# Kernel optimization log

Measured on AMD Instinct MI355X. Metric: run time of the kernel, lower is better.

## Reference

```python
import jax, jax.numpy as jnp
import numpy as np

T = 512        # sequence / max_length
I = 512        # input_dim
H = 1024       # hidden_size
O = 1          # output_size
L = 512        # max_length (attention logits)


def setup_inputs() -> dict:
    key = jax.random.key(0)
    ks = jax.random.split(key, 14)
    s = 0.02
    return {
        "input_seq": jax.random.normal(ks[0], (T, I), jnp.float32),
        "target_seq": jax.random.normal(ks[1], (T, O), jnp.float32),
        # encoder LSTM (input I -> hidden H), PyTorch gate order i,f,g,o
        "W_ih_e": jax.random.normal(ks[2], (4 * H, I), jnp.float32) * s,
        "W_hh_e": jax.random.normal(ks[3], (4 * H, H), jnp.float32) * s,
        "b_ih_e": jnp.zeros((4 * H,), jnp.float32),
        "b_hh_e": jnp.zeros((4 * H,), jnp.float32),
        # attention: Linear(2H -> L)
        "W_attn": jax.random.normal(ks[4], (L, 2 * H), jnp.float32) * s,
        "b_attn": jnp.zeros((L,), jnp.float32),
        # decoder LSTM (input 2H -> hidden H)
        "W_ih_d": jax.random.normal(ks[5], (4 * H, 2 * H), jnp.float32) * s,
        "W_hh_d": jax.random.normal(ks[6], (4 * H, H), jnp.float32) * s,
        "b_ih_d": jnp.zeros((4 * H,), jnp.float32),
        "b_hh_d": jnp.zeros((4 * H,), jnp.float32),
        # output Linear(H -> O)
        "W_out": jax.random.normal(ks[7], (O, H), jnp.float32) * s,
        "b_out": jnp.zeros((O,), jnp.float32),
    }


def _lstm_cell(x, h, c, Wih, Whh, bih, bhh):
    gates = Wih @ x + bih + Whh @ h + bhh          # [4H]
    i, f, g, o = jnp.split(gates, 4)
    c = jax.nn.sigmoid(f) * c + jax.nn.sigmoid(i) * jnp.tanh(g)
    h = jax.nn.sigmoid(o) * jnp.tanh(c)
    return h, c


def reference(input_seq, target_seq, W_ih_e, W_hh_e, b_ih_e, b_hh_e,
              W_attn, b_attn, W_ih_d, W_hh_d, b_ih_d, b_hh_d, W_out, b_out):
    Th = input_seq.shape[0]
    max_len = W_attn.shape[0]
    hid = W_hh_e.shape[1]

    def step(carry, xs):
        eh, ec, dh, dc, aw = carry
        x_t, i = xs
        eh, ec = _lstm_cell(x_t, eh, ec, W_ih_e, W_hh_e, b_ih_e, b_hh_e)
        energy = W_attn @ jnp.concatenate([eh, dh]) + b_attn   # [L]
        aw = aw.at[i].set(energy[i])
        aw = jax.nn.softmax(aw)                                 # re-softmaxed each step, as in source
        context = aw[i] * eh                                    # [H]
        din = jnp.concatenate([context, dh])                    # [2H]
        dh, dc = _lstm_cell(din, dh, dc, W_ih_d, W_hh_d, b_ih_d, b_hh_d)
        out_t = W_out @ dh + b_out                              # [O]
        return (eh, ec, dh, dc, aw), out_t

    z = jnp.zeros((hid,), input_seq.dtype)
    carry0 = (z, z, z, z, jnp.zeros((max_len,), input_seq.dtype))
    _, output_seq = jax.lax.scan(step, carry0, (input_seq, jnp.arange(Th)))
    return output_seq  # [T, O]
```

## Files before the change

kernel.cpp:

```cpp
#include <hip/hip_runtime.h>
#include <math.h>


#define T_STEPS 512
#define ENC_BLK 128
#define NBLK    256
#define NTHR    512
#define POLL_LIMIT 30000u

typedef float fv4 __attribute__((ext_vector_type(4)));

__device__ __forceinline__ float sigf(float x) { return 1.0f / (1.0f + expf(-x)); }

__device__ __forceinline__ void st_bypass4(float* p, float v) {
  asm volatile("global_store_dword %0, %1, off sc0 sc1"
               :: "v"(p), "v"(v) : "memory");
}

__device__ __forceinline__ bool valid4(fv4 v) {
  return __float_as_uint(v.x) != 0xAAAAAAAAu && __float_as_uint(v.y) != 0xAAAAAAAAu &&
         __float_as_uint(v.z) != 0xAAAAAAAAu && __float_as_uint(v.w) != 0xAAAAAAAAu;
}

__device__ __forceinline__ fv4 poll2(const float* p, int* okp) {
  fv4 a, b;
  int ok = 1;
  asm volatile("global_load_dwordx4 %0, %1, off sc0 sc1" : "=v"(a) : "v"(p) : "memory");
  for (unsigned it = 0;; ++it) {
    asm volatile("global_load_dwordx4 %0, %1, off sc0 sc1" : "=v"(b) : "v"(p) : "memory");
    asm volatile("s_waitcnt vmcnt(1)" : "+v"(a) :: "memory");
    if (valid4(a)) { asm volatile("s_waitcnt vmcnt(0)" ::: "memory"); break; }
    asm volatile("global_load_dwordx4 %0, %1, off sc0 sc1" : "=v"(a) : "v"(p) : "memory");
    asm volatile("s_waitcnt vmcnt(1)" : "+v"(b) :: "memory");
    if (valid4(b)) { asm volatile("s_waitcnt vmcnt(0)" ::: "memory"); a = b; break; }
    if (it > POLL_LIMIT) { ok = 0; asm volatile("s_waitcnt vmcnt(0)" ::: "memory"); break; }
  }
  *okp = ok;
  return a;
}

__global__ __launch_bounds__(256) void prep_gemm(const float* __restrict__ X,
                                                 const float* __restrict__ Wih,
                                                 const float* __restrict__ bih,
                                                 const float* __restrict__ bhh,
                                                 float* __restrict__ px) {
  __shared__ float Ws[64][68];
  __shared__ float Xs[64][68];
  const int r0 = blockIdx.x * 64;
  const int t0 = blockIdx.y * 64;
  const int tid = threadIdx.x;
  const int tr = tid & 15;
  const int tc = tid >> 4;
  float acc[4][4] = {{0.f}};
  for (int k0 = 0; k0 < 512; k0 += 64) {
    __syncthreads();
    const int lr = tid >> 4;
    const int lc = (tid & 15) * 4;
#pragma unroll
    for (int rep = 0; rep < 4; rep++) {
      const int row = lr + rep * 16;
      const float4 wv = *(const float4*)&Wih[(size_t)(r0 + row) * 512 + k0 + lc];
      Ws[lc + 0][row] = wv.x; Ws[lc + 1][row] = wv.y;
      Ws[lc + 2][row] = wv.z; Ws[lc + 3][row] = wv.w;
      const float4 xv = *(const float4*)&X[(size_t)(t0 + row) * 512 + k0 + lc];
      Xs[row][lc + 0] = xv.x; Xs[row][lc + 1] = xv.y;
      Xs[row][lc + 2] = xv.z; Xs[row][lc + 3] = xv.w;
    }
    __syncthreads();
    for (int kk = 0; kk < 64; kk++) {
      float a[4], x[4];
#pragma unroll
      for (int i = 0; i < 4; i++) a[i] = Ws[kk][tr * 4 + i];
#pragma unroll
      for (int j = 0; j < 4; j++) x[j] = Xs[tc * 4 + j][kk];
#pragma unroll
      for (int i = 0; i < 4; i++)
#pragma unroll
        for (int j = 0; j < 4; j++) acc[i][j] += a[i] * x[j];
    }
  }
#pragma unroll
  for (int i = 0; i < 4; i++) {
    const int r = r0 + tr * 4 + i;
    const int g = r >> 10, h = r & 1023;
    const float bsum = bih[r] + bhh[r];
#pragma unroll
    for (int j = 0; j < 4; j++) {
      const int t = t0 + tc * 4 + j;
      px[((size_t)t * 1024 + h) * 4 + g] = acc[i][j] + bsum;
    }
  }
}

__global__ __launch_bounds__(512, 1) void lstm_persist(
    const float* __restrict__ Whhe, const float* __restrict__ Wattn,
    const float* __restrict__ battn, const float* __restrict__ Wihd,
    const float* __restrict__ Whhd, const float* __restrict__ bihd,
    const float* __restrict__ bhhd, const float* __restrict__ Wout,
    const float* __restrict__ bout, const float* __restrict__ px,
    float* ehbuf, float* dhbuf, float* out) {
  __shared__ float4 xbuf[256];
  __shared__ float4 dbuf[256];
  __shared__ float  aw[512];
  __shared__ float  GA[32];
  __shared__ float  GB[32];
  __shared__ float  bd[32];
  __shared__ float  redE[4];
  __shared__ float  redE2[4];
  __shared__ float  red[8];
  __shared__ float  red2[4];
  __shared__ int    sbad;

  const int b    = blockIdx.x;
  const int tid  = threadIdx.x;
  const int w    = tid >> 6;
  const int lane = tid & 63;
  const int ri   = lane & 3;
  const int s16  = lane >> 2;
  const int g    = w >> 1;
  const int j    = ((w & 1) << 2) + ri;

  if (b < ENC_BLK) {
    const int e = b;
    const int r = (g << 10) + (e << 3) + j;
    float4 we[16];
#pragma unroll
    for (int k = 0; k < 16; k++) {
      const int m = (k + s16) & 15;
      we[k] = *(const float4*)&Whhe[(size_t)r * 1024 + s16 * 64 + m * 4];
    }
    if (tid < 256) xbuf[tid] = make_float4(0.f, 0.f, 0.f, 0.f);
    if (tid == 0) sbad = 0;
    float ec = 0.f;
    __syncthreads();

    for (int t = 0; t < T_STEPS; t++) {
      float ge = 0.f;
#pragma unroll
      for (int k = 0; k < 16; k++) {
        const int m = (k + s16) & 15;
        const float4 x = xbuf[s16 * 16 + m];
        ge += we[k].x * x.x + we[k].y * x.y + we[k].z * x.z + we[k].w * x.w;
      }
      if (s16 == 0) ge += px[((size_t)t * 1024 + (e << 3) + j) * 4 + g];
      ge += __shfl_xor(ge, 4, 64);
      ge += __shfl_xor(ge, 8, 64);
      ge += __shfl_xor(ge, 16, 64);
      ge += __shfl_xor(ge, 32, 64);
      if (lane < 4) GA[w * 4 + lane] = ge;
      __syncthreads();
      if (tid < 8) {
        const float gi = GA[tid], gf = GA[8 + tid], gg = GA[16 + tid], go = GA[24 + tid];
        const float c = sigf(gf) * ec + sigf(gi) * tanhf(gg);
        ec = c;
        const float h = sigf(go) * tanhf(c);
        st_bypass4(&ehbuf[(size_t)t * 1024 + (e << 3) + tid], h);
      }
      int ok = 1;
      if (tid < 256) {
        const fv4 ev = poll2(&ehbuf[(size_t)t * 1024 + tid * 4], &ok);
        xbuf[tid] = make_float4(ev.x, ev.y, ev.z, ev.w);
      }
      if (!ok) sbad = 1;
      __syncthreads();
      if (sbad) break;
    }
  } else {
    const int d = b - ENC_BLK;
    const int r = (g << 10) + (d << 3) + j;
    float4 w1[16], wr[16];
#pragma unroll
    for (int k = 0; k < 16; k++) {
      const int m = (k + s16) & 15;
      w1[k] = *(const float4*)&Wihd[(size_t)r * 2048 + s16 * 64 + m * 4];
      const float4 a = *(const float4*)&Wihd[(size_t)r * 2048 + 1024 + s16 * 64 + m * 4];
      const float4 c = *(const float4*)&Whhd[(size_t)r * 1024 + s16 * 64 + m * 4];
      wr[k] = make_float4(a.x + c.x, a.y + c.y, a.z + c.z, a.w + c.w);
    }
    if (tid < 32) {
      const int gg2 = tid >> 3, jj2 = tid & 7;
      bd[tid] = bihd[(gg2 << 10) + (d << 3) + jj2] + bhhd[(gg2 << 10) + (d << 3) + jj2];
    }
    aw[tid] = 0.f;
    if (tid < 256) {
      xbuf[tid] = make_float4(0.f, 0.f, 0.f, 0.f);
      dbuf[tid] = make_float4(0.f, 0.f, 0.f, 0.f);
    }
    if (tid == 0) sbad = 0;
    float dc = 0.f;
    float4 wo = make_float4(0.f, 0.f, 0.f, 0.f);
    if (tid < 256) wo = *(const float4*)&Wout[tid * 4];
    const float boutv = bout[0];
    __syncthreads();

    bool failed = false;
    for (int t = 0; t < T_STEPS; t++) {
      const float battn_t = battn[t];
      const float ex0 = expf(aw[tid]);
      float so = (tid == t) ? 0.f : ex0;
#pragma unroll
      for (int mk = 1; mk <= 32; mk <<= 1) so += __shfl_xor(so, mk, 64);
      if (lane == 0) red[w] = so;

      float4 wae = make_float4(0.f, 0.f, 0.f, 0.f);
      float4 wad = make_float4(0.f, 0.f, 0.f, 0.f);
      float epe = 0.f;
      int ok1 = 1;
      if (tid < 256) {
        wae = *(const float4*)&Wattn[(size_t)t * 2048 + tid * 4];
        wad = *(const float4*)&Wattn[(size_t)t * 2048 + 1024 + tid * 4];
        const fv4 ev = poll2(&ehbuf[(size_t)t * 1024 + tid * 4], &ok1);
        epe = wae.x * ev.x + wae.y * ev.y + wae.z * ev.z + wae.w * ev.w;
        xbuf[tid] = make_float4(ev.x, ev.y, ev.z, ev.w);
      }
      if (!ok1) sbad = 1;
#pragma unroll
      for (int mk = 1; mk <= 32; mk <<= 1) epe += __shfl_xor(epe, mk, 64);
      if (lane == 0 && w < 4) redE[w] = epe;
      __syncthreads();
      if (sbad) { failed = true; break; }

      float g1 = 0.f;
#pragma unroll
      for (int k = 0; k < 16; k++) {
        const int m = (k + s16) & 15;
        const float4 x = xbuf[s16 * 16 + m];
        g1 += w1[k].x * x.x + w1[k].y * x.y + w1[k].z * x.z + w1[k].w * x.w;
      }
      g1 += __shfl_xor(g1, 4, 64);
      g1 += __shfl_xor(g1, 8, 64);
      g1 += __shfl_xor(g1, 16, 64);
      g1 += __shfl_xor(g1, 32, 64);
      if (lane < 4) GA[w * 4 + lane] = g1;

      float epd = 0.f;
      int ok2 = 1;
      if (t > 0 && tid < 256) {
        const fv4 dv = poll2(&dhbuf[(size_t)(t - 1) * 1024 + tid * 4], &ok2);
        epd = wad.x * dv.x + wad.y * dv.y + wad.z * dv.z + wad.w * dv.w;
        dbuf[tid] = make_float4(dv.x, dv.y, dv.z, dv.w);
      }
      if (!ok2) sbad = 1;
#pragma unroll
      for (int mk = 1; mk <= 32; mk <<= 1) epd += __shfl_xor(epd, mk, 64);
      if (lane == 0 && w < 4) redE2[w] = epd;
      __syncthreads();
      if (sbad) { failed = true; break; }

      float g2 = 0.f;
#pragma unroll
      for (int k = 0; k < 16; k++) {
        const int m = (k + s16) & 15;
        const float4 dd = dbuf[s16 * 16 + m];
        g2 += wr[k].x * dd.x + wr[k].y * dd.y + wr[k].z * dd.z + wr[k].w * dd.w;
      }
      g2 += __shfl_xor(g2, 4, 64);
      g2 += __shfl_xor(g2, 8, 64);
      g2 += __shfl_xor(g2, 16, 64);
      g2 += __shfl_xor(g2, 32, 64);
      if (lane < 4) GB[w * 4 + lane] = g2;

      const float e_t = redE[0] + redE[1] + redE[2] + redE[3] +
                        redE2[0] + redE2[1] + redE2[2] + redE2[3] + battn_t;
      const float exden = expf(e_t);
      const float inv = 1.f / (red[0] + red[1] + red[2] + red[3] +
                               red[4] + red[5] + red[6] + red[7] + exden);
      const float awt = exden * inv;
      aw[tid] = ((tid == t) ? exden : ex0) * inv;
      __syncthreads();

      if (tid < 8) {
        const float gi = awt * GA[tid]      + GB[tid]      + bd[tid];
        const float gf = awt * GA[8 + tid]  + GB[8 + tid]  + bd[8 + tid];
        const float gg = awt * GA[16 + tid] + GB[16 + tid] + bd[16 + tid];
        const float go = awt * GA[24 + tid] + GB[24 + tid] + bd[24 + tid];
        const float c = sigf(gf) * dc + sigf(gi) * tanhf(gg);
        dc = c;
        const float h = sigf(go) * tanhf(c);
        st_bypass4(&dhbuf[(size_t)t * 1024 + (d << 3) + tid], h);
      }
    }

    if (!failed) {
#pragma unroll
      for (int i = 0; i < 4; i++) {
        const int t = d * 4 + i;
        float op = 0.f;
        int ok = 1;
        if (tid < 256) {
          const fv4 dv = poll2(&dhbuf[(size_t)t * 1024 + tid * 4], &ok);
          op = wo.x * dv.x + wo.y * dv.y + wo.z * dv.z + wo.w * dv.w;
        }
        if (!ok) break;
#pragma unroll
        for (int mk = 1; mk <= 32; mk <<= 1) op += __shfl_xor(op, mk, 64);
        if (lane == 0 && w < 4) red2[w] = op;
        __syncthreads();
        if (tid == 0) out[t] = red2[0] + red2[1] + red2[2] + red2[3] + boutv;
        __syncthreads();
      }
    }
  }
}

extern "C" void kernel_launch(void* const* d_in, const int* in_sizes, int n_in,
                              void* d_out, int out_size, void* d_ws, size_t ws_size,
                              hipStream_t stream) {
  const float* X     = (const float*)d_in[0];
  const float* Wihe  = (const float*)d_in[2];
  const float* Whhe  = (const float*)d_in[3];
  const float* bihe  = (const float*)d_in[4];
  const float* bhhe  = (const float*)d_in[5];
  const float* Wattn = (const float*)d_in[6];
  const float* battn = (const float*)d_in[7];
  const float* Wihd  = (const float*)d_in[8];
  const float* Whhd  = (const float*)d_in[9];
  const float* bihd  = (const float*)d_in[10];
  const float* bhhd  = (const float*)d_in[11];
  const float* Wo    = (const float*)d_in[12];
  const float* bo    = (const float*)d_in[13];
  float* out = (float*)d_out;

  float* ws    = (float*)d_ws;
  float* px    = ws;
  float* ehbuf = px + (size_t)T_STEPS * 1024 * 4;
  float* dhbuf = ehbuf + (size_t)T_STEPS * 1024;
  const size_t need = ((size_t)T_STEPS * 1024 * 6) * sizeof(float);
  if (ws_size < need) return;

  prep_gemm<<<dim3(64, 8), 256, 0, stream>>>(X, Wihe, bihe, bhhe, px);
  lstm_persist<<<NBLK, NTHR, 0, stream>>>(
      Whhe, Wattn, battn, Wihd, Whhd, bihd, bhhd, Wo, bo, px, ehbuf, dhbuf, out);
}
```

Before: 1.999 ms.

## Relay hidden states through per-XCD local replicas to cut cross-die polling latency

Measured after the change: 2.248 ms. 1.12x slower.

```diff
diff --git a/kernel.cpp b/kernel.cpp
--- a/kernel.cpp
+++ b/kernel.cpp
@@ -7,14 +7,21 @@
 #define NBLK    256
 #define NTHR    512
 #define POLL_LIMIT 30000u
+#define LOC_LIMIT  1024u
+#define REPSZ ((size_t)T_STEPS * 1024)
 
 typedef float fv4 __attribute__((ext_vector_type(4)));
 
 __device__ __forceinline__ float sigf(float x) { return 1.0f / (1.0f + expf(-x)); }
 
-__device__ __forceinline__ void st_bypass4(float* p, float v) {
-  asm volatile("global_store_dword %0, %1, off sc0 sc1"
-               :: "v"(p), "v"(v) : "memory");
+__device__ __forceinline__ void st_llc4(float* p, float v) {
+  asm volatile("global_store_dword %0, %1, off sc0 sc1" :: "v"(p), "v"(v) : "memory");
+}
+__device__ __forceinline__ void st_loc4(float* p, float v) {
+  asm volatile("global_store_dword %0, %1, off sc0" :: "v"(p), "v"(v) : "memory");
+}
+__device__ __forceinline__ void st_loc16(float* p, fv4 v) {
+  asm volatile("global_store_dwordx4 %0, %1, off sc0" :: "v"(p), "v"(v) : "memory");
 }
 
 __device__ __forceinline__ bool valid4(fv4 v) {
@@ -22,7 +29,7 @@
          __float_as_uint(v.z) != 0xAAAAAAAAu && __float_as_uint(v.w) != 0xAAAAAAAAu;
 }
 
-__device__ __forceinline__ fv4 poll2(const float* p, int* okp) {
+__device__ __forceinline__ fv4 poll2_llc(const float* p, unsigned limit, int* okp) {
   fv4 a, b;
   int ok = 1;
   asm volatile("global_load_dwordx4 %0, %1, off sc0 sc1" : "=v"(a) : "v"(p) : "memory");
@@ -33,17 +40,45 @@
     asm volatile("global_load_dwordx4 %0, %1, off sc0 sc1" : "=v"(a) : "v"(p) : "memory");
     asm volatile("s_waitcnt vmcnt(1)" : "+v"(b) :: "memory");
     if (valid4(b)) { asm volatile("s_waitcnt vmcnt(0)" ::: "memory"); a = b; break; }
-    if (it > POLL_LIMIT) { ok = 0; asm volatile("s_waitcnt vmcnt(0)" ::: "memory"); break; }
+    if (it > limit) { ok = 0; asm volatile("s_waitcnt vmcnt(0)" ::: "memory"); break; }
   }
   *okp = ok;
   return a;
+}
+__device__ __forceinline__ fv4 poll2_loc(const float* p, unsigned limit, int* okp) {
+  fv4 a, b;
+  int ok = 1;
+  asm volatile("global_load_dwordx4 %0, %1, off sc0" : "=v"(a) : "v"(p) : "memory");
+  for (unsigned it = 0;; ++it) {
+    asm volatile("global_load_dwordx4 %0, %1, off sc0" : "=v"(b) : "v"(p) : "memory");
+    asm volatile("s_waitcnt vmcnt(1)" : "+v"(a) :: "memory");
+    if (valid4(a)) { asm volatile("s_waitcnt vmcnt(0)" ::: "memory"); break; }
+    asm volatile("global_load_dwordx4 %0, %1, off sc0" : "=v"(a) : "v"(p) : "memory");
+    asm volatile("s_waitcnt vmcnt(1)" : "+v"(b) :: "memory");
+    if (valid4(b)) { asm volatile("s_waitcnt vmcnt(0)" ::: "memory"); a = b; break; }
+    if (it > limit) { ok = 0; asm volatile("s_waitcnt vmcnt(0)" ::: "memory"); break; }
+  }
+  *okp = ok;
+  return a;
+}
+__device__ __forceinline__ fv4 poll_any(const float* ploc, const float* pllc,
+                                        int* sfall, int* okp) {
+  if (!*sfall) {
+    int ok1;
+    const fv4 v = poll2_loc(ploc, LOC_LIMIT, &ok1);
+    if (ok1) { *okp = 1; return v; }
+    *sfall = 1;
+  }
+  return poll2_llc(pllc, POLL_LIMIT, okp);
 }
 
 __global__ __launch_bounds__(256) void prep_gemm(const float* __restrict__ X,
                                                  const float* __restrict__ Wih,
                                                  const float* __restrict__ bih,
                                                  const float* __restrict__ bhh,
-                                                 float* __restrict__ px) {
+                                                 float* __restrict__ px,
+                                                 int* ctrs) {
+  if (blockIdx.x == 0 && blockIdx.y == 0 && threadIdx.x < 16) ctrs[threadIdx.x] = 0;
   __shared__ float Ws[64][68];
   __shared__ float Xs[64][68];
   const int r0 = blockIdx.x * 64;
@@ -98,7 +133,8 @@
     const float* __restrict__ Whhd, const float* __restrict__ bihd,
     const float* __restrict__ bhhd, const float* __restrict__ Wout,
     const float* __restrict__ bout, const float* __restrict__ px,
-    float* ehbuf, float* dhbuf, float* out) {
+    float* ehbuf, float* dhbuf, float* ehloc, float* dhloc, int* ctrs,
+    int use_loc, float* out) {
   __shared__ float4 xbuf[256];
   __shared__ float4 dbuf[256];
   __shared__ float  aw[512];
@@ -110,6 +146,9 @@
   __shared__ float  red[8];
   __shared__ float  red2[4];
   __shared__ int    sbad;
+  __shared__ int    s_slot;
+  __shared__ int    sfallE;
+  __shared__ int    sfallD;
 
   const int b    = blockIdx.x;
   const int tid  = threadIdx.x;
@@ -120,6 +159,20 @@
   const int g    = w >> 1;
   const int j    = ((w & 1) << 2) + ri;
 
+  __builtin_amdgcn_fence(__ATOMIC_ACQUIRE, "agent");
+  unsigned xcd;
+  asm volatile("s_getreg_b32 %0, hwreg(HW_REG_XCC_ID)" : "=s"(xcd));
+  xcd &= 7u;
+  if (tid == 0) {
+    sbad = 0;
+    sfallE = use_loc ? 0 : 1;
+    sfallD = use_loc ? 0 : 1;
+    int* ctr = (b < ENC_BLK) ? &ctrs[xcd] : &ctrs[8 + xcd];
+    s_slot = use_loc ? atomicAdd(ctr, 1) : 1;
+  }
+  float* myeloc = ehloc + (size_t)xcd * REPSZ;
+  float* mydloc = dhloc + (size_t)xcd * REPSZ;
+
   if (b < ENC_BLK) {
     const int e = b;
     const int r = (g << 10) + (e << 3) + j;
@@ -130,9 +183,9 @@
       we[k] = *(const float4*)&Whhe[(size_t)r * 1024 + s16 * 64 + m * 4];
     }
     if (tid < 256) xbuf[tid] = make_float4(0.f, 0.f, 0.f, 0.f);
-    if (tid == 0) sbad = 0;
     float ec = 0.f;
     __syncthreads();
+    const bool relay = (s_slot == 0);
 
     for (int t = 0; t < T_STEPS; t++) {
       float ge = 0.f;
@@ -154,11 +207,19 @@
         const float c = sigf(gf) * ec + sigf(gi) * tanhf(gg);
         ec = c;
         const float h = sigf(go) * tanhf(c);
-        st_bypass4(&ehbuf[(size_t)t * 1024 + (e << 3) + tid], h);
+        st_llc4(&ehbuf[(size_t)t * 1024 + (e << 3) + tid], h);
+        if (use_loc) st_loc4(&myeloc[(size_t)t * 1024 + (e << 3) + tid], h);
       }
       int ok = 1;
       if (tid < 256) {
-        const fv4 ev = poll2(&ehbuf[(size_t)t * 1024 + tid * 4], &ok);
+        const float* pllc = &ehbuf[(size_t)t * 1024 + tid * 4];
+        fv4 ev;
+        if (relay && use_loc) {
+          ev = poll2_llc(pllc, POLL_LIMIT, &ok);
+          st_loc16(&myeloc[(size_t)t * 1024 + tid * 4], ev);
+        } else {
+          ev = poll_any(&myeloc[(size_t)t * 1024 + tid * 4], pllc, &sfallE, &ok);
+        }
         xbuf[tid] = make_float4(ev.x, ev.y, ev.z, ev.w);
       }
       if (!ok) sbad = 1;
@@ -186,12 +247,12 @@
       xbuf[tid] = make_float4(0.f, 0.f, 0.f, 0.f);
       dbuf[tid] = make_float4(0.f, 0.f, 0.f, 0.f);
     }
-    if (tid == 0) sbad = 0;
     float dc = 0.f;
     float4 wo = make_float4(0.f, 0.f, 0.f, 0.f);
     if (tid < 256) wo = *(const float4*)&Wout[tid * 4];
     const float boutv = bout[0];
     __syncthreads();
+    const bool relay = (s_slot == 0);
 
     bool failed = false;
     for (int t = 0; t < T_STEPS; t++) {
@@ -209,7 +270,8 @@
       if (tid < 256) {
         wae = *(const float4*)&Wattn[(size_t)t * 2048 + tid * 4];
         wad = *(const float4*)&Wattn[(size_t)t * 2048 + 1024 + tid * 4];
-        const fv4 ev = poll2(&ehbuf[(size_t)t * 1024 + tid * 4], &ok1);
+        const fv4 ev = poll_any(&myeloc[(size_t)t * 1024 + tid * 4],
+                                &ehbuf[(size_t)t * 1024 + tid * 4], &sfallE, &ok1);
         epe = wae.x * ev.x + wae.y * ev.y + wae.z * ev.z + wae.w * ev.w;
         xbuf[tid] = make_float4(ev.x, ev.y, ev.z, ev.w);
       }
@@ -236,7 +298,14 @@
       float epd = 0.f;
       int ok2 = 1;
       if (t > 0 && tid < 256) {
-        const fv4 dv = poll2(&dhbuf[(size_t)(t - 1) * 1024 + tid * 4], &ok2);
+        const float* pllc = &dhbuf[(size_t)(t - 1) * 1024 + tid * 4];
+        fv4 dv;
+        if (relay && use_loc) {
+          dv = poll2_llc(pllc, POLL_LIMIT, &ok2);
+          st_loc16(&mydloc[(size_t)(t - 1) * 1024 + tid * 4], dv);
+        } else {
+          dv = poll_any(&mydloc[(size_t)(t - 1) * 1024 + tid * 4], pllc, &sfallD, &ok2);
+        }
         epd = wad.x * dv.x + wad.y * dv.y + wad.z * dv.z + wad.w * dv.w;
         dbuf[tid] = make_float4(dv.x, dv.y, dv.z, dv.w);
       }
@@ -277,7 +346,8 @@
         const float c = sigf(gf) * dc + sigf(gi) * tanhf(gg);
         dc = c;
         const float h = sigf(go) * tanhf(c);
-        st_bypass4(&dhbuf[(size_t)t * 1024 + (d << 3) + tid], h);
+        st_llc4(&dhbuf[(size_t)t * 1024 + (d << 3) + tid], h);
+        if (use_loc) st_loc4(&mydloc[(size_t)t * 1024 + (d << 3) + tid], h);
       }
     }
 
@@ -288,7 +358,7 @@
         float op = 0.f;
         int ok = 1;
         if (tid < 256) {
-          const fv4 dv = poll2(&dhbuf[(size_t)t * 1024 + tid * 4], &ok);
+          const fv4 dv = poll2_llc(&dhbuf[(size_t)t * 1024 + tid * 4], POLL_LIMIT, &ok);
           op = wo.x * dv.x + wo.y * dv.y + wo.z * dv.z + wo.w * dv.w;
         }
         if (!ok) break;
@@ -324,11 +394,18 @@
   float* ws    = (float*)d_ws;
   float* px    = ws;
   float* ehbuf = px + (size_t)T_STEPS * 1024 * 4;
-  float* dhbuf = ehbuf + (size_t)T_STEPS * 1024;
-  const size_t need = ((size_t)T_STEPS * 1024 * 6) * sizeof(float);
-  if (ws_size < need) return;
-
-  prep_gemm<<<dim3(64, 8), 256, 0, stream>>>(X, Wihe, bihe, bhhe, px);
+  float* dhbuf = ehbuf + REPSZ;
+  int*   ctrs  = (int*)(dhbuf + REPSZ);
+  float* ehloc = (float*)(ctrs + 16);
+  float* dhloc = ehloc + 8 * REPSZ;
+
+  const size_t need_min  = ((size_t)T_STEPS * 1024 * 6) * sizeof(float) + 16 * sizeof(int);
+  const size_t need_full = need_min + 16 * REPSZ * sizeof(float);
+  if (ws_size < need_min) return;
+  const int use_loc = (ws_size >= need_full) ? 1 : 0;
+
+  prep_gemm<<<dim3(64, 8), 256, 0, stream>>>(X, Wihe, bihe, bhhe, px, ctrs);
   lstm_persist<<<NBLK, NTHR, 0, stream>>>(
-      Whhe, Wattn, battn, Wihd, Whhd, bihd, bhhd, Wo, bo, px, ehbuf, dhbuf, out);
-}
+      Whhe, Wattn, battn, Wihd, Whhd, bihd, bhhd, Wo, bo, px, ehbuf, dhbuf,
+      ehloc, dhloc, ctrs, use_loc, out);
+}
```
